# Performance work log

Hardware: AMD Instinct MI355X
Metric: run time of the kernel (lower is better)

## Reference

```python
import jax, jax.numpy as jnp
import numpy as np

T, H, I, E, K = 4096, 2048, 4096, 8, 2

def setup_inputs() -> dict:
    key = jax.random.key(0)
    k1, k2, k3, k4, k5 = jax.random.split(key, 5)
    return {
        "hidden_states": jax.random.normal(k1, (T, H), dtype=jnp.float32),
        "topk_weights": jax.random.uniform(k2, (T, K), dtype=jnp.float32, minval=0.01, maxval=1.0),
        "topk_ids": jax.random.randint(k3, (T, K), 0, E, dtype=jnp.int64),
        "gate_up_weights": jax.random.normal(k4, (E, 2 * I, H), dtype=jnp.float32) * 0.02,
        "down_weights": jax.random.normal(k5, (E, H, I), dtype=jnp.float32) * 0.02,
    }

def reference(hidden_states, topk_weights, topk_ids, gate_up_weights, down_weights):
    # renormalize=True: per-token top-k weights sum to 1
    tw = topk_weights / jnp.sum(topk_weights, axis=-1, keepdims=True)  # [T, K]
    n_experts = gate_up_weights.shape[0]
    # per-expert combine weight for each token: sum of tw where routed to expert e -> [E, T]
    expert_w = jax.vmap(
        lambda e: jnp.sum(jnp.where(topk_ids == e, tw, 0.0), axis=-1)
    )(jnp.arange(n_experts))

    def body(acc, ew):
        gu, dw, w = ew  # gu: [2I, H], dw: [H, I], w: [T]
        h = hidden_states @ gu.T            # [T, 2I]
        gate, up = jnp.split(h, 2, axis=-1)  # silu_and_mul epilogue
        act = jax.nn.silu(gate) * up        # [T, I]
        out_e = act @ dw.T                  # [T, H]
        return acc + w[:, None] * out_e, None

    init = jnp.zeros_like(hidden_states)
    out, _ = jax.lax.scan(body, init, (gate_up_weights, down_weights, expert_w))
    return out
```

## Files before the change

### kernel.cpp

```cpp
#include <hip/hip_runtime.h>


#define T_TOK 4096
#define H_DIM 2048
#define I_DIM 4096
#define E_NUM 8
#define K_TOP 2
#define NSLOT (T_TOK * K_TOP)

#define BM 128
#define BN 128
#define BK 32
#define LDKO 72

typedef float f32x4 __attribute__((ext_vector_type(4)));
typedef __bf16 bf16x8 __attribute__((ext_vector_type(8)));
typedef unsigned int u32x4 __attribute__((ext_vector_type(4)));

static __device__ __forceinline__ unsigned short f2bf(float f) {
  unsigned u = __float_as_uint(f);
  u += 0x7FFFu + ((u >> 16) & 1u);
  return (unsigned short)(u >> 16);
}

static __device__ __forceinline__ unsigned long long pack4bf(float x0, float x1, float x2, float x3) {
  unsigned lo = (unsigned)f2bf(x0) | ((unsigned)f2bf(x1) << 16);
  unsigned hi = (unsigned)f2bf(x2) | ((unsigned)f2bf(x3) << 16);
  return (unsigned long long)lo | ((unsigned long long)hi << 32);
}

static __device__ __forceinline__ void gload16(void* lds, const void* g) {
  __builtin_amdgcn_global_load_lds(
      (const __attribute__((address_space(1))) unsigned int*)(g),
      (__attribute__((address_space(3))) unsigned int*)(lds), 16, 0, 0);
}

__global__ void routing_kernel(const float* __restrict__ tw,
                               const int* __restrict__ ids,
                               int* __restrict__ offsets,
                               int* __restrict__ stok,
                               float* __restrict__ sw,
                               int* __restrict__ slot_of) {
  __shared__ int cnt[E_NUM];
  __shared__ int cur[E_NUM];
  __shared__ int basesh[E_NUM + 1];
  int tid = threadIdx.x;
  if (tid < E_NUM) cnt[tid] = 0;
  __syncthreads();
  for (int idx = tid; idx < NSLOT; idx += 256) atomicAdd(&cnt[ids[idx]], 1);
  __syncthreads();
  if (tid == 0) {
    int acc = 0;
    for (int e = 0; e < E_NUM; ++e) { basesh[e] = acc; acc += cnt[e]; }
    basesh[E_NUM] = acc;
    for (int e = 0; e <= E_NUM; ++e) offsets[e] = basesh[e];
  }
  __syncthreads();
  if (tid < E_NUM) cur[tid] = basesh[tid];
  __syncthreads();
  for (int idx = tid; idx < NSLOT; idx += 256) {
    int t = idx >> 1;
    float w0 = tw[t * 2], w1 = tw[t * 2 + 1];
    float w = ((idx & 1) ? w1 : w0) / (w0 + w1);
    int e = ids[idx];
    int slot = atomicAdd(&cur[e], 1);
    stok[slot] = t;
    sw[slot] = w;
    slot_of[idx] = slot;
  }
}

__global__ __launch_bounds__(256) void cvt_bf16_kernel(const float* __restrict__ in,
                                                       unsigned short* __restrict__ out,
                                                       long long n8) {
  long long stride = (long long)gridDim.x * 256;
  for (long long i = (long long)blockIdx.x * 256 + threadIdx.x; i < n8; i += stride) {
    long long o = i * 8;
    f32x4 v0 = *(const f32x4*)(in + o);
    f32x4 v1 = *(const f32x4*)(in + o + 4);
    unsigned long long p0 = pack4bf(v0[0], v0[1], v0[2], v0[3]);
    unsigned long long p1 = pack4bf(v1[0], v1[1], v1[2], v1[3]);
    u32x4 st;
    st[0] = (unsigned)p0; st[1] = (unsigned)(p0 >> 32);
    st[2] = (unsigned)p1; st[3] = (unsigned)(p1 >> 32);
    *(u32x4*)(out + o) = st;
  }
}

__global__ __launch_bounds__(256, 2) void gemm1_bf16_kernel(
    const unsigned short* __restrict__ hb,
    const unsigned short* __restrict__ gub,
    const int* __restrict__ offsets, const int* __restrict__ stok,
    unsigned short* __restrict__ act) {
  int e = blockIdx.z;
  int base = offsets[e];
  int cnt = offsets[e + 1] - base;
  int m0 = blockIdx.y * BM;
  if (m0 >= cnt) return;
  int n0 = blockIdx.x * BN;
  int rem = cnt - m0;

  __shared__ __attribute__((aligned(16))) unsigned short As[2][BM * BK];
  __shared__ __attribute__((aligned(16))) unsigned short Bg[2][BN * BK];
  __shared__ __attribute__((aligned(16))) unsigned short Bu[2][BN * BK];
  __shared__ int toks[BM];

  int tid = threadIdx.x;
  if (tid < BM) toks[tid] = (tid < rem) ? stok[base + m0 + tid] : stok[base];
  __syncthreads();

  int lane = tid & 63;
  int wid = tid >> 6;
  int sr = lane >> 2;
  int scz = (((lane & 3) ^ ((lane >> 3) & 3)) << 3);

  const unsigned short* wrow = gub + (size_t)e * (2 * (size_t)I_DIM) * H_DIM;
  const unsigned short* pa[2];
  const unsigned short* pg[2];
  const unsigned short* pu[2];
  int lb[2];
#pragma unroll
  for (int s = 0; s < 2; ++s) {
    int grp = (wid * 2 + s) * 16;
    int row = grp + sr;
    pa[s] = hb + (size_t)toks[row] * H_DIM + scz;
    pg[s] = wrow + (size_t)(n0 + row) * H_DIM + scz;
    pu[s] = wrow + (size_t)(I_DIM + n0 + row) * H_DIM + scz;
    lb[s] = grp * BK;
  }

  int lm = lane & 15;
  int q = lane >> 4;
  int wm = (wid >> 1) * 64;
  int wn = (wid & 1) * 64;
  int rcs = ((q ^ ((lm >> 1) & 3)) << 3);

  f32x4 accg[4][4] = {};
  f32x4 accu[4][4] = {};

#pragma unroll
  for (int s = 0; s < 2; ++s) {
    gload16(&As[0][lb[s]], pa[s]);
    gload16(&Bg[0][lb[s]], pg[s]);
    gload16(&Bu[0][lb[s]], pu[s]);
  }
  __syncthreads();

  int cur = 0;
  for (int kb = 0; kb < H_DIM; kb += BK) {
    if (kb + BK < H_DIM) {
      int nk = kb + BK;
#pragma unroll
      for (int s = 0; s < 2; ++s) {
        gload16(&As[cur ^ 1][lb[s]], pa[s] + nk);
        gload16(&Bg[cur ^ 1][lb[s]], pg[s] + nk);
        gload16(&Bu[cur ^ 1][lb[s]], pu[s] + nk);
      }
    }
    bf16x8 a[4], bg[4], bu[4];
#pragma unroll
    for (int i = 0; i < 4; ++i)
      a[i] = *(const bf16x8*)&As[cur][(wm + i * 16 + lm) * BK + rcs];
#pragma unroll
    for (int j = 0; j < 4; ++j) {
      bg[j] = *(const bf16x8*)&Bg[cur][(wn + j * 16 + lm) * BK + rcs];
      bu[j] = *(const bf16x8*)&Bu[cur][(wn + j * 16 + lm) * BK + rcs];
    }
    __builtin_amdgcn_s_setprio(1);
#pragma unroll
    for (int i = 0; i < 4; ++i)
#pragma unroll
      for (int j = 0; j < 4; ++j) {
        accg[i][j] = __builtin_amdgcn_mfma_f32_16x16x32_bf16(a[i], bg[j], accg[i][j], 0, 0, 0);
        accu[i][j] = __builtin_amdgcn_mfma_f32_16x16x32_bf16(a[i], bu[j], accu[i][j], 0, 0, 0);
      }
    __builtin_amdgcn_s_setprio(0);
    __syncthreads();
    cur ^= 1;
  }

#pragma unroll
  for (int i = 0; i < 4; ++i) {
    int mb = wm + i * 16 + q * 4;
#pragma unroll
    for (int r = 0; r < 4; ++r) {
      int m = mb + r;
      if (m < rem) {
        size_t rowoff = (size_t)(base + m0 + m) * I_DIM + n0;
#pragma unroll
        for (int j = 0; j < 4; ++j) {
          int n = wn + j * 16 + lm;
          float g = accg[i][j][r];
          float u = accu[i][j][r];
          float aa = (g / (1.0f + __expf(-g))) * u;
          act[rowoff + n] = f2bf(aa);
        }
      }
    }
  }
}

__global__ __launch_bounds__(256, 2) void gemm2_bf16_kernel(
    const unsigned short* __restrict__ act, const unsigned short* __restrict__ dwb,
    const int* __restrict__ offsets, const float* __restrict__ sw,
    float* __restrict__ dout) {
  int e = blockIdx.z;
  int base = offsets[e];
  int cnt = offsets[e + 1] - base;
  int m0 = blockIdx.y * BM;
  if (m0 >= cnt) return;
  int n0 = blockIdx.x * BN;
  int rem = cnt - m0;

  __shared__ __attribute__((aligned(16))) unsigned short As[2][BM * BK];
  __shared__ __attribute__((aligned(16))) unsigned short Bs[2][BN * BK];
  __shared__ float wsl[BM];

  int tid = threadIdx.x;
  if (tid < BM) wsl[tid] = (tid < rem) ? sw[base + m0 + tid] : 0.f;

  int lane = tid & 63;
  int wid = tid >> 6;
  int sr = lane >> 2;
  int scz = (((lane & 3) ^ ((lane >> 3) & 3)) << 3);

  const unsigned short* dp = dwb + (size_t)e * ((size_t)H_DIM * I_DIM);
  const unsigned short* pa[2];
  const unsigned short* pb[2];
  int lb[2];
#pragma unroll
  for (int s = 0; s < 2; ++s) {
    int grp = (wid * 2 + s) * 16;
    int row = grp + sr;
    pa[s] = act + (size_t)(base + m0 + row) * I_DIM + scz;
    pb[s] = dp + (size_t)(n0 + row) * I_DIM + scz;
    lb[s] = grp * BK;
  }

  int lm = lane & 15;
  int q = lane >> 4;
  int wm = (wid >> 1) * 64;
  int wn = (wid & 1) * 64;
  int rcs = ((q ^ ((lm >> 1) & 3)) << 3);

  f32x4 acc[4][4] = {};

#pragma unroll
  for (int s = 0; s < 2; ++s) {
    gload16(&As[0][lb[s]], pa[s]);
    gload16(&Bs[0][lb[s]], pb[s]);
  }
  __syncthreads();

  int cur = 0;
  for (int kb = 0; kb < I_DIM; kb += BK) {
    if (kb + BK < I_DIM) {
      int nk = kb + BK;
#pragma unroll
      for (int s = 0; s < 2; ++s) {
        gload16(&As[cur ^ 1][lb[s]], pa[s] + nk);
        gload16(&Bs[cur ^ 1][lb[s]], pb[s] + nk);
      }
    }
    bf16x8 a[4], b[4];
#pragma unroll
    for (int i = 0; i < 4; ++i)
      a[i] = *(const bf16x8*)&As[cur][(wm + i * 16 + lm) * BK + rcs];
#pragma unroll
    for (int j = 0; j < 4; ++j)
      b[j] = *(const bf16x8*)&Bs[cur][(wn + j * 16 + lm) * BK + rcs];
    __builtin_amdgcn_s_setprio(1);
#pragma unroll
    for (int i = 0; i < 4; ++i)
#pragma unroll
      for (int j = 0; j < 4; ++j)
        acc[i][j] = __builtin_amdgcn_mfma_f32_16x16x32_bf16(a[i], b[j], acc[i][j], 0, 0, 0);
    __builtin_amdgcn_s_setprio(0);
    __syncthreads();
    cur ^= 1;
  }

#pragma unroll
  for (int i = 0; i < 4; ++i) {
    int mb = wm + i * 16 + q * 4;
#pragma unroll
    for (int r = 0; r < 4; ++r) {
      int m = mb + r;
      if (m < rem) {
        float w = wsl[m];
        size_t rowoff = (size_t)(base + m0 + m) * H_DIM + n0;
#pragma unroll
        for (int j = 0; j < 4; ++j)
          dout[rowoff + wn + j * 16 + lm] = acc[i][j][r] * w;
      }
    }
  }
}

__global__ __launch_bounds__(256, 2) void gemm1_kernel(
    const float* __restrict__ hidden, const float* __restrict__ gu,
    const int* __restrict__ offsets, const int* __restrict__ stok,
    unsigned short* __restrict__ act) {
  int e = blockIdx.z;
  int base = offsets[e];
  int cnt = offsets[e + 1] - base;
  int m0 = blockIdx.y * BM;
  if (m0 >= cnt) return;
  int n0 = blockIdx.x * BN;
  int rem = cnt - m0;

  __shared__ unsigned short As[BM * LDKO];
  __shared__ unsigned short Bg[BM * LDKO];
  __shared__ unsigned short Bu[BM * LDKO];
  __shared__ int toks[BM];

  int tid = threadIdx.x;
  if (tid < BM) toks[tid] = (tid < rem) ? stok[base + m0 + tid] : -1;
  __syncthreads();

  int lane = tid & 63;
  int wid = tid >> 6;
  int wm = (wid >> 1) * 64;
  int wn = (wid & 1) * 64;
  int lm = lane & 15;
  int q = lane >> 4;

  f32x4 accg[4][4] = {};
  f32x4 accu[4][4] = {};
  const float* gup = gu + (size_t)e * (2 * (size_t)I_DIM * H_DIM);

  for (int kb = 0; kb < H_DIM; kb += 64) {
#pragma unroll
    for (int s = 0; s < 8; ++s) {
      int task = tid + s * 256;
      int row = task >> 4;
      int cg = (task & 15) << 2;
      int tok = toks[row];
      float x0 = 0.f, x1 = 0.f, x2 = 0.f, x3 = 0.f;
      if (tok >= 0) {
        f32x4 v = *(const f32x4*)(hidden + (size_t)tok * H_DIM + kb + cg);
        x0 = v[0]; x1 = v[1]; x2 = v[2]; x3 = v[3];
      }
      *(unsigned long long*)&As[row * LDKO + cg] = pack4bf(x0, x1, x2, x3);
    }
#pragma unroll
    for (int s = 0; s < 8; ++s) {
      int task = tid + s * 256;
      int row = task >> 4;
      int cg = (task & 15) << 2;
      f32x4 vg = *(const f32x4*)(gup + (size_t)(n0 + row) * H_DIM + kb + cg);
      f32x4 vu = *(const f32x4*)(gup + (size_t)(I_DIM + n0 + row) * H_DIM + kb + cg);
      *(unsigned long long*)&Bg[row * LDKO + cg] = pack4bf(vg[0], vg[1], vg[2], vg[3]);
      *(unsigned long long*)&Bu[row * LDKO + cg] = pack4bf(vu[0], vu[1], vu[2], vu[3]);
    }
    __syncthreads();
#pragma unroll
    for (int ks = 0; ks < 2; ++ks) {
      int ko = ks * 32 + q * 8;
      bf16x8 a[4], bg[4], bu[4];
#pragma unroll
      for (int i = 0; i < 4; ++i)
        a[i] = *(const bf16x8*)&As[(wm + i * 16 + lm) * LDKO + ko];
#pragma unroll
      for (int j = 0; j < 4; ++j) {
        bg[j] = *(const bf16x8*)&Bg[(wn + j * 16 + lm) * LDKO + ko];
        bu[j] = *(const bf16x8*)&Bu[(wn + j * 16 + lm) * LDKO + ko];
      }
#pragma unroll
      for (int i = 0; i < 4; ++i)
#pragma unroll
        for (int j = 0; j < 4; ++j) {
          accg[i][j] = __builtin_amdgcn_mfma_f32_16x16x32_bf16(a[i], bg[j], accg[i][j], 0, 0, 0);
          accu[i][j] = __builtin_amdgcn_mfma_f32_16x16x32_bf16(a[i], bu[j], accu[i][j], 0, 0, 0);
        }
    }
    __syncthreads();
  }

#pragma unroll
  for (int i = 0; i < 4; ++i) {
    int mb = wm + i * 16 + q * 4;
#pragma unroll
    for (int r = 0; r < 4; ++r) {
      int m = mb + r;
      if (m < rem) {
        size_t rowoff = (size_t)(base + m0 + m) * I_DIM + n0;
#pragma unroll
        for (int j = 0; j < 4; ++j) {
          int n = wn + j * 16 + lm;
          float g = accg[i][j][r];
          float u = accu[i][j][r];
          float aa = (g / (1.0f + __expf(-g))) * u;
          act[rowoff + n] = f2bf(aa);
        }
      }
    }
  }
}

__global__ __launch_bounds__(256, 2) void gemm2_kernel(
    const unsigned short* __restrict__ act, const float* __restrict__ dwn,
    const int* __restrict__ offsets, const float* __restrict__ sw,
    float* __restrict__ dout) {
  int e = blockIdx.z;
  int base = offsets[e];
  int cnt = offsets[e + 1] - base;
  int m0 = blockIdx.y * BM;
  if (m0 >= cnt) return;
  int n0 = blockIdx.x * BN;
  int rem = cnt - m0;

  __shared__ unsigned short As[BM * LDKO];
  __shared__ unsigned short Bs[BM * LDKO];
  __shared__ float wsl[BM];

  int tid = threadIdx.x;
  if (tid < BM) wsl[tid] = (tid < rem) ? sw[base + m0 + tid] : 0.f;

  int lane = tid & 63;
  int wid = tid >> 6;
  int wm = (wid >> 1) * 64;
  int wn = (wid & 1) * 64;
  int lm = lane & 15;
  int q = lane >> 4;

  f32x4 acc[4][4] = {};
  const float* dp = dwn + (size_t)e * ((size_t)H_DIM * I_DIM);
  const unsigned short* ap = act + (size_t)(base + m0) * I_DIM;

  for (int kb = 0; kb < I_DIM; kb += 64) {
#pragma unroll
    for (int s = 0; s < 4; ++s) {
      int task = tid + s * 256;
      int row = task >> 3;
      int cg = (task & 7) << 3;
      u32x4 v = *(const u32x4*)(ap + (size_t)row * I_DIM + kb + cg);
      *(u32x4*)&As[row * LDKO + cg] = v;
    }
#pragma unroll
    for (int s = 0; s < 8; ++s) {
      int task = tid + s * 256;
      int row = task >> 4;
      int cg = (task & 15) << 2;
      f32x4 v = *(const f32x4*)(dp + (size_t)(n0 + row) * I_DIM + kb + cg);
      *(unsigned long long*)&Bs[row * LDKO + cg] = pack4bf(v[0], v[1], v[2], v[3]);
    }
    __syncthreads();
#pragma unroll
    for (int ks = 0; ks < 2; ++ks) {
      int ko = ks * 32 + q * 8;
      bf16x8 a[4], b[4];
#pragma unroll
      for (int i = 0; i < 4; ++i)
        a[i] = *(const bf16x8*)&As[(wm + i * 16 + lm) * LDKO + ko];
#pragma unroll
      for (int j = 0; j < 4; ++j)
        b[j] = *(const bf16x8*)&Bs[(wn + j * 16 + lm) * LDKO + ko];
#pragma unroll
      for (int i = 0; i < 4; ++i)
#pragma unroll
        for (int j = 0; j < 4; ++j)
          acc[i][j] = __builtin_amdgcn_mfma_f32_16x16x32_bf16(a[i], b[j], acc[i][j], 0, 0, 0);
    }
    __syncthreads();
  }

#pragma unroll
  for (int i = 0; i < 4; ++i) {
    int mb = wm + i * 16 + q * 4;
#pragma unroll
    for (int r = 0; r < 4; ++r) {
      int m = mb + r;
      if (m < rem) {
        float w = wsl[m];
        size_t rowoff = (size_t)(base + m0 + m) * H_DIM + n0;
#pragma unroll
        for (int j = 0; j < 4; ++j)
          dout[rowoff + wn + j * 16 + lm] = acc[i][j][r] * w;
      }
    }
  }
}

__global__ void combine_kernel(const f32x4* __restrict__ dout4,
                               const int* __restrict__ slot_of,
                               f32x4* __restrict__ out4) {
  int idx = blockIdx.x * 256 + threadIdx.x;
  int t = idx >> 9;
  int c = idx & 511;
  int s0 = slot_of[t * 2];
  int s1 = slot_of[t * 2 + 1];
  f32x4 r = dout4[(size_t)s0 * 512 + c] + dout4[(size_t)s1 * 512 + c];
  out4[idx] = r;
}

extern "C" void kernel_launch(void* const* d_in, const int* in_sizes, int n_in,
                              void* d_out, int out_size, void* d_ws, size_t ws_size,
                              hipStream_t stream) {
  const float* hidden = (const float*)d_in[0];
  const float* tw     = (const float*)d_in[1];
  const int*   ids    = (const int*)d_in[2];
  const float* gu     = (const float*)d_in[3];
  const float* dwn    = (const float*)d_in[4];
  float* out = (float*)d_out;
  char* ws = (char*)d_ws;

  int*   offsets = (int*)ws;
  int*   stok    = (int*)(ws + 256);
  float* swp     = (float*)(ws + 256 + 32768);
  int*   slot_of = (int*)(ws + 256 + 65536);
  const size_t base_off = 1 << 17;
  const size_t act_sz   = (size_t)(NSLOT + BM) * I_DIM * 2;

  routing_kernel<<<1, 256, 0, stream>>>(tw, ids, offsets, stok, swp, slot_of);

  const size_t hb_sz  = (size_t)T_TOK * H_DIM * 2;
  const size_t gu_sz  = (size_t)E_NUM * 2 * (size_t)I_DIM * H_DIM * 2;
  const size_t dwn_sz = (size_t)E_NUM * (size_t)H_DIM * I_DIM * 2;
  const size_t w_off  = base_off + hb_sz;
  const size_t need   = w_off + gu_sz + act_sz;

  if (ws_size >= need) {
    unsigned short* hb   = (unsigned short*)(ws + base_off);
    unsigned short* gub  = (unsigned short*)(ws + w_off);
    unsigned short* dwb  = (unsigned short*)(ws + w_off);
    float*          dout = (float*)(ws + w_off + dwn_sz);
    unsigned short* act  = (unsigned short*)(ws + w_off + gu_sz);

    cvt_bf16_kernel<<<4096, 256, 0, stream>>>(hidden, hb, (long long)T_TOK * H_DIM / 8);
    cvt_bf16_kernel<<<8192, 256, 0, stream>>>(gu, gub, (long long)E_NUM * 2 * I_DIM * H_DIM / 8);
    gemm1_bf16_kernel<<<dim3(I_DIM / BN, NSLOT / BM, E_NUM), 256, 0, stream>>>(hb, gub, offsets, stok, act);
    cvt_bf16_kernel<<<8192, 256, 0, stream>>>(dwn, dwb, (long long)E_NUM * H_DIM * I_DIM / 8);
    gemm2_bf16_kernel<<<dim3(H_DIM / BN, NSLOT / BM, E_NUM), 256, 0, stream>>>(act, dwb, offsets, swp, dout);
    combine_kernel<<<(T_TOK * H_DIM / 4) / 256, 256, 0, stream>>>((const f32x4*)dout, slot_of, (f32x4*)out);
  } else {
    unsigned short* act  = (unsigned short*)(ws + base_off);
    float*          dout = (float*)(ws + base_off + act_sz);
    gemm1_kernel<<<dim3(I_DIM / BN, NSLOT / BM, E_NUM), 256, 0, stream>>>(hidden, gu, offsets, stok, act);
    gemm2_kernel<<<dim3(H_DIM / BN, NSLOT / BM, E_NUM), 256, 0, stream>>>(act, dwn, offsets, swp, dout);
    combine_kernel<<<(T_TOK * H_DIM / 4) / 256, 256, 0, stream>>>((const f32x4*)dout, slot_of, (f32x4*)out);
  }
}
```

Measured before the change: 1.586 ms.

## Triple-buffer LDS in MoE GEMMs with vmcnt-based waits and single barrier

Both bf16 grouped GEMMs move from double-buffered to triple-buffered shared-memory staging, issuing loads two K-steps ahead. Explicit s_waitcnt vmcnt waits replace the trailing __syncthreads, leaving one barrier per iteration. The goal is to hide global-load latency behind the MFMA work. gemm2's launch bounds are raised to 3 blocks per CU, and the conversion kernels run with fewer grid blocks. In exchange, LDS use grows by half, which may limit occupancy in gemm1, and the hand-written vmcnt counts depend on how gload16 lowers to instructions.

```diff
diff --git a/kernel.cpp b/kernel.cpp
--- a/kernel.cpp
+++ b/kernel.cpp
@@ -100,9 +100,9 @@
   int n0 = blockIdx.x * BN;
   int rem = cnt - m0;
 
-  __shared__ __attribute__((aligned(16))) unsigned short As[2][BM * BK];
-  __shared__ __attribute__((aligned(16))) unsigned short Bg[2][BN * BK];
-  __shared__ __attribute__((aligned(16))) unsigned short Bu[2][BN * BK];
+  __shared__ __attribute__((aligned(16))) unsigned short As[3][BM * BK];
+  __shared__ __attribute__((aligned(16))) unsigned short Bg[3][BN * BK];
+  __shared__ __attribute__((aligned(16))) unsigned short Bu[3][BN * BK];
   __shared__ int toks[BM];
 
   int tid = threadIdx.x;
@@ -138,46 +138,54 @@
   f32x4 accg[4][4] = {};
   f32x4 accu[4][4] = {};
 
-#pragma unroll
-  for (int s = 0; s < 2; ++s) {
-    gload16(&As[0][lb[s]], pa[s]);
-    gload16(&Bg[0][lb[s]], pg[s]);
-    gload16(&Bu[0][lb[s]], pu[s]);
-  }
-  __syncthreads();
+  auto stage = [&](int b, int kbo) {
+#pragma unroll
+    for (int s = 0; s < 2; ++s) {
+      gload16(&As[b][lb[s]], pa[s] + kbo);
+      gload16(&Bg[b][lb[s]], pg[s] + kbo);
+      gload16(&Bu[b][lb[s]], pu[s] + kbo);
+    }
+  };
+  auto compute = [&](int b) {
+    bf16x8 a[4], bgf[4], buf_[4];
+#pragma unroll
+    for (int i = 0; i < 4; ++i)
+      a[i] = *(const bf16x8*)&As[b][(wm + i * 16 + lm) * BK + rcs];
+#pragma unroll
+    for (int j = 0; j < 4; ++j) {
+      bgf[j] = *(const bf16x8*)&Bg[b][(wn + j * 16 + lm) * BK + rcs];
+      buf_[j] = *(const bf16x8*)&Bu[b][(wn + j * 16 + lm) * BK + rcs];
+    }
+    __builtin_amdgcn_s_setprio(1);
+#pragma unroll
+    for (int i = 0; i < 4; ++i)
+#pragma unroll
+      for (int j = 0; j < 4; ++j) {
+        accg[i][j] = __builtin_amdgcn_mfma_f32_16x16x32_bf16(a[i], bgf[j], accg[i][j], 0, 0, 0);
+        accu[i][j] = __builtin_amdgcn_mfma_f32_16x16x32_bf16(a[i], buf_[j], accu[i][j], 0, 0, 0);
+      }
+    __builtin_amdgcn_s_setprio(0);
+  };
+
+  stage(0, 0);
+  stage(1, BK);
 
   int cur = 0;
-  for (int kb = 0; kb < H_DIM; kb += BK) {
-    if (kb + BK < H_DIM) {
-      int nk = kb + BK;
-#pragma unroll
-      for (int s = 0; s < 2; ++s) {
-        gload16(&As[cur ^ 1][lb[s]], pa[s] + nk);
-        gload16(&Bg[cur ^ 1][lb[s]], pg[s] + nk);
-        gload16(&Bu[cur ^ 1][lb[s]], pu[s] + nk);
-      }
-    }
-    bf16x8 a[4], bg[4], bu[4];
-#pragma unroll
-    for (int i = 0; i < 4; ++i)
-      a[i] = *(const bf16x8*)&As[cur][(wm + i * 16 + lm) * BK + rcs];
-#pragma unroll
-    for (int j = 0; j < 4; ++j) {
-      bg[j] = *(const bf16x8*)&Bg[cur][(wn + j * 16 + lm) * BK + rcs];
-      bu[j] = *(const bf16x8*)&Bu[cur][(wn + j * 16 + lm) * BK + rcs];
-    }
-    __builtin_amdgcn_s_setprio(1);
-#pragma unroll
-    for (int i = 0; i < 4; ++i)
-#pragma unroll
-      for (int j = 0; j < 4; ++j) {
-        accg[i][j] = __builtin_amdgcn_mfma_f32_16x16x32_bf16(a[i], bg[j], accg[i][j], 0, 0, 0);
-        accu[i][j] = __builtin_amdgcn_mfma_f32_16x16x32_bf16(a[i], bu[j], accu[i][j], 0, 0, 0);
-      }
-    __builtin_amdgcn_s_setprio(0);
-    __syncthreads();
-    cur ^= 1;
-  }
+  for (int kb = 0; kb < H_DIM - 2 * BK; kb += BK) {
+    asm volatile("s_waitcnt vmcnt(6)" ::: "memory");
+    __builtin_amdgcn_s_barrier();
+    int nxt = cur + 2; if (nxt >= 3) nxt -= 3;
+    stage(nxt, kb + 2 * BK);
+    compute(cur);
+    cur = (cur + 1 == 3) ? 0 : cur + 1;
+  }
+  asm volatile("s_waitcnt vmcnt(6)" ::: "memory");
+  __builtin_amdgcn_s_barrier();
+  compute(cur);
+  cur = (cur + 1 == 3) ? 0 : cur + 1;
+  asm volatile("s_waitcnt vmcnt(0)" ::: "memory");
+  __builtin_amdgcn_s_barrier();
+  compute(cur);
 
 #pragma unroll
   for (int i = 0; i < 4; ++i) {
@@ -200,7 +208,7 @@
   }
 }
 
-__global__ __launch_bounds__(256, 2) void gemm2_bf16_kernel(
+__global__ __launch_bounds__(256, 3) void gemm2_bf16_kernel(
     const unsigned short* __restrict__ act, const unsigned short* __restrict__ dwb,
     const int* __restrict__ offsets, const float* __restrict__ sw,
     float* __restrict__ dout) {
@@ -212,12 +220,13 @@
   int n0 = blockIdx.x * BN;
   int rem = cnt - m0;
 
-  __shared__ __attribute__((aligned(16))) unsigned short As[2][BM * BK];
-  __shared__ __attribute__((aligned(16))) unsigned short Bs[2][BN * BK];
+  __shared__ __attribute__((aligned(16))) unsigned short As[3][BM * BK];
+  __shared__ __attribute__((aligned(16))) unsigned short Bs[3][BN * BK];
   __shared__ float wsl[BM];
 
   int tid = threadIdx.x;
   if (tid < BM) wsl[tid] = (tid < rem) ? sw[base + m0 + tid] : 0.f;
+  __syncthreads();
 
   int lane = tid & 63;
   int wid = tid >> 6;
@@ -245,40 +254,49 @@
 
   f32x4 acc[4][4] = {};
 
-#pragma unroll
-  for (int s = 0; s < 2; ++s) {
-    gload16(&As[0][lb[s]], pa[s]);
-    gload16(&Bs[0][lb[s]], pb[s]);
-  }
-  __syncthreads();
+  auto stage = [&](int b, int kbo) {
+#pragma unroll
+    for (int s = 0; s < 2; ++s) {
+      gload16(&As[b][lb[s]], pa[s] + kbo);
+      gload16(&Bs[b][lb[s]], pb[s] + kbo);
+    }
+  };
+  auto compute = [&](int b) {
+    bf16x8 a[4], bf[4];
+#pragma unroll
+    for (int i = 0; i < 4; ++i)
+      a[i] = *(const bf16x8*)&As[b][(wm + i * 16 + lm) * BK + rcs];
+#pragma unroll
+    for (int j = 0; j < 4; ++j)
+      bf[j] = *(const bf16x8*)&Bs[b][(wn + j * 16 + lm) * BK + rcs];
+    __builtin_amdgcn_s_setprio(1);
+#pragma unroll
+    for (int i = 0; i < 4; ++i)
+#pragma unroll
+      for (int j = 0; j < 4; ++j)
+        acc[i][j] = __builtin_amdgcn_mfma_f32_16x16x32_bf16(a[i], bf[j], acc[i][j], 0, 0, 0);
+    __builtin_amdgcn_s_setprio(0);
+  };
+
+  stage(0, 0);
+  stage(1, BK);
 
   int cur = 0;
-  for (int kb = 0; kb < I_DIM; kb += BK) {
-    if (kb + BK < I_DIM) {
-      int nk = kb + BK;
-#pragma unroll
-      for (int s = 0; s < 2; ++s) {
-        gload16(&As[cur ^ 1][lb[s]], pa[s] + nk);
-        gload16(&Bs[cur ^ 1][lb[s]], pb[s] + nk);
-      }
-    }
-    bf16x8 a[4], b[4];
-#pragma unroll
-    for (int i = 0; i < 4; ++i)
-      a[i] = *(const bf16x8*)&As[cur][(wm + i * 16 + lm) * BK + rcs];
-#pragma unroll
-    for (int j = 0; j < 4; ++j)
-      b[j] = *(const bf16x8*)&Bs[cur][(wn + j * 16 + lm) * BK + rcs];
-    __builtin_amdgcn_s_setprio(1);
-#pragma unroll
-    for (int i = 0; i < 4; ++i)
-#pragma unroll
-      for (int j = 0; j < 4; ++j)
-        acc[i][j] = __builtin_amdgcn_mfma_f32_16x16x32_bf16(a[i], b[j], acc[i][j], 0, 0, 0);
-    __builtin_amdgcn_s_setprio(0);
-    __syncthreads();
-    cur ^= 1;
-  }
+  for (int kb = 0; kb < I_DIM - 2 * BK; kb += BK) {
+    asm volatile("s_waitcnt vmcnt(4)" ::: "memory");
+    __builtin_amdgcn_s_barrier();
+    int nxt = cur + 2; if (nxt >= 3) nxt -= 3;
+    stage(nxt, kb + 2 * BK);
+    compute(cur);
+    cur = (cur + 1 == 3) ? 0 : cur + 1;
+  }
+  asm volatile("s_waitcnt vmcnt(4)" ::: "memory");
+  __builtin_amdgcn_s_barrier();
+  compute(cur);
+  cur = (cur + 1 == 3) ? 0 : cur + 1;
+  asm volatile("s_waitcnt vmcnt(0)" ::: "memory");
+  __builtin_amdgcn_s_barrier();
+  compute(cur);
 
 #pragma unroll
   for (int i = 0; i < 4; ++i) {
@@ -527,10 +545,10 @@
     float*          dout = (float*)(ws + w_off + dwn_sz);
     unsigned short* act  = (unsigned short*)(ws + w_off + gu_sz);
 
-    cvt_bf16_kernel<<<4096, 256, 0, stream>>>(hidden, hb, (long long)T_TOK * H_DIM / 8);
-    cvt_bf16_kernel<<<8192, 256, 0, stream>>>(gu, gub, (long long)E_NUM * 2 * I_DIM * H_DIM / 8);
+    cvt_bf16_kernel<<<2048, 256, 0, stream>>>(hidden, hb, (long long)T_TOK * H_DIM / 8);
+    cvt_bf16_kernel<<<2048, 256, 0, stream>>>(gu, gub, (long long)E_NUM * 2 * I_DIM * H_DIM / 8);
     gemm1_bf16_kernel<<<dim3(I_DIM / BN, NSLOT / BM, E_NUM), 256, 0, stream>>>(hb, gub, offsets, stok, act);
-    cvt_bf16_kernel<<<8192, 256, 0, stream>>>(dwn, dwb, (long long)E_NUM * H_DIM * I_DIM / 8);
+    cvt_bf16_kernel<<<2048, 256, 0, stream>>>(dwn, dwb, (long long)E_NUM * H_DIM * I_DIM / 8);
     gemm2_bf16_kernel<<<dim3(H_DIM / BN, NSLOT / BM, E_NUM), 256, 0, stream>>>(act, dwb, offsets, swp, dout);
     combine_kernel<<<(T_TOK * H_DIM / 4) / 256, 256, 0, stream>>>((const f32x4*)dout, slot_of, (f32x4*)out);
   } else {
```

After: 1.565 ms. No clear change (-1.3%).
